# Performance work log

Hardware: AMD Instinct MI355X
Metric: run time of the kernel (lower is better)

## Reference

```python
import jax, jax.numpy as jnp
import numpy as np

H, KV, D, EPS = 32, 8, 128, 1e-6
G = H // KV  # kv groups = 4
ROPE_THETA = 5000000.0


def _rms_norm(x, gamma):
    # x: (..., D)
    return x * jax.lax.rsqrt(jnp.mean(x * x, axis=-1, keepdims=True) + EPS) * gamma


def _rotate_half(x):
    x1, x2 = jnp.split(x, 2, axis=-1)
    return jnp.concatenate([-x2, x1], axis=-1)


def _apply_rope(x, cos, sin):
    # x: (b, h, s, D); cos/sin: (b, s, 1, D) -> (b, 1, s, D)
    cos = jnp.transpose(cos, (0, 2, 1, 3))
    sin = jnp.transpose(sin, (0, 2, 1, 3))
    return x * cos + _rotate_half(x) * sin


def setup_inputs() -> dict:
    key = jax.random.key(0)
    ks = jax.random.split(key, 8)
    b, s, hid = 2, 2048, 2560
    hidden = jax.random.normal(ks[0], (b, s, hid), dtype=jnp.float32)
    # realistic RoPE tables (half-split convention matching _rotate_half)
    inv_freq = 1.0 / (ROPE_THETA ** (np.arange(0, D, 2, dtype=np.float32) / D))  # (D/2,)
    pos = np.arange(s, dtype=np.float32)
    freqs = np.outer(pos, inv_freq)                     # (s, D/2)
    emb = np.concatenate([freqs, freqs], axis=-1)       # (s, D)
    cos = jnp.broadcast_to(jnp.asarray(np.cos(emb))[None, :, None, :], (b, s, 1, D))
    sin = jnp.broadcast_to(jnp.asarray(np.sin(emb))[None, :, None, :], (b, s, 1, D))
    sc = 1.0 / np.sqrt(hid)
    wq = jax.random.normal(ks[1], (H * D, hid), dtype=jnp.float32) * sc
    wk = jax.random.normal(ks[2], (KV * D, hid), dtype=jnp.float32) * sc
    wv = jax.random.normal(ks[3], (KV * D, hid), dtype=jnp.float32) * sc
    wo = jax.random.normal(ks[4], (hid, H * D), dtype=jnp.float32) * (1.0 / np.sqrt(H * D))
    q_gamma = jnp.ones((D,), dtype=jnp.float32)
    k_gamma = jnp.ones((D,), dtype=jnp.float32)
    return {"hidden": hidden, "cos": cos, "sin": sin, "wq": wq, "wk": wk,
            "wv": wv, "wo": wo, "q_gamma": q_gamma, "k_gamma": k_gamma}


def reference(hidden, cos, sin, wq, wk, wv, wo, q_gamma, k_gamma):
    b, s, _ = hidden.shape
    # projections -> (b, heads, s, D)
    q = (hidden @ wq.T).reshape(b, s, H, D).transpose(0, 2, 1, 3)
    k = (hidden @ wk.T).reshape(b, s, KV, D).transpose(0, 2, 1, 3)
    v = (hidden @ wv.T).reshape(b, s, KV, D).transpose(0, 2, 1, 3)
    # QK-RMSNorm over head_dim
    q = _rms_norm(q, q_gamma)
    k = _rms_norm(k, k_gamma)
    # RoPE
    q = _apply_rope(q, cos, sin)
    k = _apply_rope(k, cos, sin)
    new_k, new_v = k, v  # kv cache (no prior cache)
    # GQA attention without materializing expanded K/V
    qg = q.reshape(b, KV, G, s, D)
    scale = 1.0 / np.sqrt(D)
    scores = jnp.einsum('bkgqd,bkld->bkgql', qg, k) * scale  # (b,KV,G,s,s)
    causal = jnp.tril(jnp.ones((s, s), dtype=bool))
    scores = jnp.where(causal, scores, jnp.finfo(scores.dtype).min)
    probs = jax.nn.softmax(scores, axis=-1)
    out = jnp.einsum('bkgql,bkld->bkgqd', probs, v)          # (b,KV,G,s,D)
    out = out.reshape(b, H, s, D).transpose(0, 2, 1, 3).reshape(b, s, H * D)
    return (out @ wo.T, new_k, new_v)
```

## Files before the change

### kernel.cpp

```cpp
#include <hip/hip_runtime.h>
#include <stdint.h>

typedef unsigned short u16;
typedef __attribute__((ext_vector_type(8))) short short8;
typedef __attribute__((ext_vector_type(4))) float f32x4;

#define MFMA_BF16(a,b,c) __builtin_amdgcn_mfma_f32_16x16x32_bf16((a),(b),(c),0,0,0)

#define S_BARRIER()  asm volatile("s_barrier" ::: "memory")
#define WAIT_LGKM0() asm volatile("s_waitcnt lgkmcnt(0)" ::: "memory")
#define WAIT_VM(N)   asm volatile("s_waitcnt vmcnt(" #N ")" ::: "memory")

__device__ __forceinline__ u16 f2bf(float x) {
    uint32_t u = __builtin_bit_cast(uint32_t, x);
    u += 0x7fffu + ((u >> 16) & 1u);
    return (u16)(u >> 16);
}
__device__ __forceinline__ float bf2f(u16 u) {
    return __builtin_bit_cast(float, (uint32_t)u << 16);
}
__device__ __forceinline__ void glds16(const void* g, void* lds) {
    __builtin_amdgcn_global_load_lds((const __attribute__((address_space(1))) void*)g,
                                     (__attribute__((address_space(3))) void*)lds,
                                     16, 0, 0);
}

__device__ __forceinline__ void cvt4(const float* __restrict__ s,
                                     u16* __restrict__ d, int i) {
    float4 v = *(const float4*)(s + i);
    ushort4 o;
    o.x = f2bf(v.x); o.y = f2bf(v.y); o.z = f2bf(v.z); o.w = f2bf(v.w);
    *(ushort4*)(d + i) = o;
}
__global__ __launch_bounds__(256) void cvt_all(
        const float* __restrict__ s0, u16* __restrict__ d0,
        const float* __restrict__ s1, u16* __restrict__ d1,
        const float* __restrict__ s2, u16* __restrict__ d2,
        const float* __restrict__ s3, u16* __restrict__ d3,
        const float* __restrict__ s4, u16* __restrict__ d4)
{
    int i = (blockIdx.x * 256 + threadIdx.x) * 4;
    if      (i < 10485760) cvt4(s0, d0, i);
    else if (i < 20971520) cvt4(s1, d1, i - 10485760);
    else if (i < 23592960) cvt4(s2, d2, i - 20971520);
    else if (i < 26214400) cvt4(s3, d3, i - 23592960);
    else if (i < 36700160) cvt4(s4, d4, i - 26214400);
}

template<int MH, int NH>
__device__ __forceinline__ void mm16(f32x4 (&acc)[8][4],
                                     const short8 (&a)[4][2],
                                     const short8 (&b)[2][2]) {
#pragma unroll
    for (int k2 = 0; k2 < 2; k2++)
#pragma unroll
        for (int mi = 0; mi < 4; mi++)
#pragma unroll
            for (int nj = 0; nj < 2; nj++)
                acc[MH * 4 + mi][NH * 2 + nj] =
                    MFMA_BF16(a[mi][k2], b[nj][k2], acc[MH * 4 + mi][NH * 2 + nj]);
}

template<bool BF16_OUT>
__global__ __launch_bounds__(512, 2) void gemm8(const u16* __restrict__ A,
                                                const u16* __restrict__ B,
                                                void* __restrict__ Cv,
                                                int K, int lda, int ldb, int ldc,
                                                int ntn)
{
    __shared__ __align__(16) u16 Sm[65536];
    const int t = threadIdx.x;
    const int w = t >> 6, l = t & 63;
    const int lrow = l & 15, lk = l >> 4;
    const int wm = w >> 2, wn = w & 3;

    const int nwg = (int)gridDim.x;
    const int cpx = nwg >> 3;
    const int id = (int)blockIdx.x;
    const int sw = (id & 7) * cpx + (id >> 3);
    const int tm = sw / ntn, tn = sw - tm * ntn;
    const int m0 = tm * 256, n0 = tn * 256;

    const int nkt = K >> 6;
    const size_t laneOffA = (size_t)(w * 16 + (l >> 3)) * lda + (((l & 7) ^ (l >> 3)) * 8);
    const size_t laneOffB = (size_t)(w * 16 + (l >> 3)) * ldb + (((l & 7) ^ (l >> 3)) * 8);
    const u16* Ag = A + (size_t)m0 * lda;
    const u16* Bg = B + (size_t)n0 * ldb;

    auto STAGE_A = [&](int kt, int slot, int h) {
#pragma unroll
        for (int j = 0; j < 2; j++)
            glds16(Ag + laneOffA + (size_t)(h * 128 + j * 8) * lda + kt * 64,
                   (char*)Sm + slot * 65536 + h * 16384 + w * 2048 + j * 1024);
    };
    auto STAGE_B = [&](int kt, int slot, int h) {
#pragma unroll
        for (int j = 0; j < 2; j++)
            glds16(Bg + laneOffB + (size_t)(h * 128 + j * 8) * ldb + kt * 64,
                   (char*)Sm + 32768 + slot * 65536 + h * 16384 + w * 2048 + j * 1024);
    };
    auto READ_A = [&](short8 (&a)[4][2], int slot, int rb) {
#pragma unroll
        for (int mi = 0; mi < 4; mi++)
#pragma unroll
            for (int k2 = 0; k2 < 2; k2++) {
                int row = rb + mi * 16 + lrow;
                a[mi][k2] = *(const short8*)&Sm[slot * 32768 + row * 64 +
                                                (((k2 * 4 + lk) ^ (lrow & 7)) * 8)];
            }
    };
    auto READ_B = [&](short8 (&b)[2][2], int slot, int rb) {
#pragma unroll
        for (int nj = 0; nj < 2; nj++)
#pragma unroll
            for (int k2 = 0; k2 < 2; k2++) {
                int row = rb + nj * 16 + lrow;
                b[nj][k2] = *(const short8*)&Sm[slot * 32768 + 16384 + row * 64 +
                                                (((k2 * 4 + lk) ^ (lrow & 7)) * 8)];
            }
    };

    f32x4 acc[8][4];
#pragma unroll
    for (int i = 0; i < 8; i++)
#pragma unroll
        for (int j = 0; j < 4; j++) acc[i][j] = (f32x4){0.f, 0.f, 0.f, 0.f};
    short8 aF0[4][2], aF1[4][2], bF0[2][2], bF1[2][2];

    STAGE_A(0, 0, 0); STAGE_A(0, 0, 1);
    STAGE_B(0, 0, 0); STAGE_B(0, 0, 1);
    const int k1 = (nkt > 1) ? 1 : 0;
    STAGE_A(k1, 1, 0); STAGE_A(k1, 1, 1);
    WAIT_VM(4);
    S_BARRIER();

    for (int kt = 0; kt < nkt; ++kt) {
        const int slot = kt & 1, nslot = slot ^ 1;
        const int ktB = (kt + 1 < nkt) ? kt + 1 : kt;
        const int ktA = (kt + 2 < nkt) ? kt + 2 : kt;
        READ_A(aF0, slot, wm * 128);
        READ_B(bF0, slot, wn * 64);
        STAGE_B(ktB, nslot, 0);
        S_BARRIER();
        WAIT_LGKM0();
        __builtin_amdgcn_sched_barrier(0);
        __builtin_amdgcn_s_setprio(1);
        mm16<0, 0>(acc, aF0, bF0);
        __builtin_amdgcn_s_setprio(0);
        S_BARRIER();
        READ_A(aF1, slot, wm * 128 + 64);
        STAGE_B(ktB, nslot, 1);
        S_BARRIER();
        WAIT_LGKM0();
        __builtin_amdgcn_sched_barrier(0);
        __builtin_amdgcn_s_setprio(1);
        mm16<1, 0>(acc, aF1, bF0);
        __builtin_amdgcn_s_setprio(0);
        S_BARRIER();
        READ_B(bF1, slot, wn * 64 + 32);
        STAGE_A(ktA, slot, 0);
        S_BARRIER();
        WAIT_LGKM0();
        __builtin_amdgcn_sched_barrier(0);
        __builtin_amdgcn_s_setprio(1);
        mm16<1, 1>(acc, aF1, bF1);
        __builtin_amdgcn_s_setprio(0);
        S_BARRIER();
        STAGE_A(ktA, slot, 1);
        S_BARRIER();
        __builtin_amdgcn_s_setprio(1);
        mm16<0, 1>(acc, aF0, bF1);
        __builtin_amdgcn_s_setprio(0);
        WAIT_VM(4);
        S_BARRIER();
    }
    WAIT_VM(0);

#pragma unroll
    for (int mi = 0; mi < 8; mi++) {
#pragma unroll
        for (int r = 0; r < 4; r++) {
            int row = m0 + wm * 128 + mi * 16 + lk * 4 + r;
#pragma unroll
            for (int nj = 0; nj < 4; nj++) {
                int col = n0 + wn * 64 + nj * 16 + lrow;
                float v = acc[mi][nj][r];
                if (BF16_OUT) ((u16*)Cv)[(size_t)row * ldc + col] = f2bf(v);
                else          ((float*)Cv)[(size_t)row * ldc + col] = v;
            }
        }
    }
}

__global__ __launch_bounds__(256) void norm_rope_qk(const u16* __restrict__ qkv,
        const float* __restrict__ cosb, const float* __restrict__ sinb,
        const float* __restrict__ qg, const float* __restrict__ kg,
        u16* __restrict__ qb, u16* __restrict__ kb, float* __restrict__ k_out)
{
    const int idx = blockIdx.x * 4 + (threadIdx.x >> 6);
    const int l = threadIdx.x & 63;
    const int tok = idx / 40, hd = idx - tok * 40;
    const int b = tok >> 11, pos = tok & 2047;
    const u16* row = qkv + (size_t)tok * 6144 + hd * 128;
    ushort2 xr = *(const ushort2*)(row + 2 * l);
    float xa = bf2f(xr.x), xb = bf2f(xr.y);
    float ss = xa * xa + xb * xb;
#pragma unroll
    for (int m = 1; m < 64; m <<= 1) ss += __shfl_xor(ss, m, 64);
    float rn = rsqrtf(ss * (1.0f / 128.0f) + 1e-6f);

    const float* gm = (hd < 32) ? qg : kg;
    float2 g = *(const float2*)(gm + 2 * l);
    float na = xa * rn * g.x, nb = xb * rn * g.y;
    float pa = __shfl_xor(na, 32, 64);
    float pb = __shfl_xor(nb, 32, 64);
    float2 c = *(const float2*)(cosb + (size_t)tok * 128 + 2 * l);
    float2 s = *(const float2*)(sinb + (size_t)tok * 128 + 2 * l);
    float sgn = (l < 32) ? -1.0f : 1.0f;
    float ya = na * c.x + sgn * pa * s.x;
    float yb = nb * c.y + sgn * pb * s.y;
    if (hd < 32) {
        const float qs = 0.08838834764831845f;
        size_t base = (((size_t)b * 32 + hd) * 2048 + pos) * 128;
        ushort2 o; o.x = f2bf(ya * qs); o.y = f2bf(yb * qs);
        *(ushort2*)(qb + base + 2 * l) = o;
    } else {
        int kv = hd - 32;
        size_t base = (((size_t)b * 8 + kv) * 2048 + pos) * 128;
        *(float2*)(k_out + base + 2 * l) = make_float2(ya, yb);
        ushort2 o; o.x = f2bf(ya); o.y = f2bf(yb);
        *(ushort2*)(kb + base + 2 * l) = o;
    }
}

__global__ __launch_bounds__(256) void v_pack(const u16* __restrict__ qkv,
        float* __restrict__ v_out, u16* __restrict__ vtb)
{
    __shared__ __align__(16) u16 T[64 * 128];
    const int pb = blockIdx.x, bkv = blockIdx.y;
    const int b = bkv >> 3, kv = bkv & 7;
    const int p0 = pb * 64;
    const int t = threadIdx.x;
    const int pos = t >> 2, ch4 = t & 3;
    const u16* src = qkv + (size_t)(b * 2048 + p0 + pos) * 6144 + (40 + kv) * 128 + ch4 * 32;
    float* vdst = v_out + ((size_t)bkv * 2048 + p0 + pos) * 128 + ch4 * 32;
#pragma unroll
    for (int j = 0; j < 4; j++) {
        short8 x = *(const short8*)(src + j * 8);
        float4 f0, f1;
        f0.x = bf2f(x[0]); f0.y = bf2f(x[1]); f0.z = bf2f(x[2]); f0.w = bf2f(x[3]);
        f1.x = bf2f(x[4]); f1.y = bf2f(x[5]); f1.z = bf2f(x[6]); f1.w = bf2f(x[7]);
        *(float4*)(vdst + j * 8)     = f0;
        *(float4*)(vdst + j * 8 + 4) = f1;
        int slot = (ch4 * 4 + j) ^ (pos & 7);
        *(short8*)&T[pos * 128 + slot * 8] = x;
    }
    __syncthreads();
    const int d = t & 127, ph = t >> 7;
    u16* obase = vtb + ((size_t)bkv * 128 + d) * 2048 + p0 + ph * 32;
#pragma unroll
    for (int g = 0; g < 4; g++) {
        short8 tv;
#pragma unroll
        for (int jj = 0; jj < 8; jj++) {
            int pp = ph * 32 + g * 8 + jj;
            int slot = (d >> 3) ^ (pp & 7);
            tv[jj] = (short)T[pp * 128 + slot * 8 + (d & 7)];
        }
        *(short8*)(obase + g * 8) = tv;
    }
}

__global__ __launch_bounds__(256, 3) void attn_kernel(const u16* __restrict__ qb,
        const u16* __restrict__ kb, const u16* __restrict__ vtb,
        u16* __restrict__ ao)
{
    __shared__ __align__(16) u16 Ks[64 * 128];
    __shared__ __align__(16) u16 Vs[128 * 64];
    __shared__ __align__(16) u16 Ps[4][32 * 72];

    const int p = (int)blockIdx.x;
    const int g = (p & 7) + ((p >> 5) << 3);
    const int bh = g * 4 + ((p >> 3) & 3);
    const int b = bh >> 5, h = bh & 31;
    const int kvh = h >> 2;
    const int qt = (int)gridDim.y - 1 - (int)blockIdx.y;
    const int q0 = qt * 128;
    const int t = threadIdx.x, w = t >> 6, l = t & 63;
    const int lrow = l & 15, lk = l >> 4;

    const u16* qbase  = qb  + ((size_t)b * 32 + h)  * 2048 * 128;
    const u16* kbase  = kb  + ((size_t)b * 8 + kvh) * 2048 * 128;
    const u16* vtbase = vtb + ((size_t)b * 8 + kvh) * 128 * 2048;

    short8 qf[2][4];
#pragma unroll
    for (int m = 0; m < 2; m++) {
        const u16* qrow = qbase + (size_t)(q0 + w * 32 + m * 16 + lrow) * 128 + lk * 8;
#pragma unroll
        for (int ks = 0; ks < 4; ks++) qf[m][ks] = *(const short8*)(qrow + ks * 32);
    }

    f32x4 o[2][8];
#pragma unroll
    for (int m = 0; m < 2; m++)
#pragma unroll
        for (int i = 0; i < 8; i++) o[m][i] = (f32x4){0.f, 0.f, 0.f, 0.f};
    float lsum[2][4] = {{0.f,0.f,0.f,0.f},{0.f,0.f,0.f,0.f}};

    int kR[4], kG[4], vR[4], vG[4];
#pragma unroll
    for (int i = 0; i < 4; i++) {
        int c = i * 256 + t;
        kR[i] = c >> 4; kG[i] = (c & 15) ^ (kR[i] & 7);
        vR[i] = c >> 3; vG[i] = (c & 7)  ^ (vR[i] & 7);
    }
    char* Ksb = (char*)Ks + w * 1024;
    char* Vsb = (char*)Vs + w * 1024;
    u16* pw = &Ps[w][0];
    const int wrow_max = q0 + w * 32 + 31;

    const int nkt = 2 * qt + 2;
    for (int kt = 0; kt < nkt; kt++) {
        const int kv0 = kt * 64;
        __syncthreads();
#pragma unroll
        for (int i = 0; i < 4; i++)
            glds16(kbase + (size_t)(kv0 + kR[i]) * 128 + kG[i] * 8, Ksb + i * 4096);
#pragma unroll
        for (int i = 0; i < 4; i++)
            glds16(vtbase + (size_t)vR[i] * 2048 + kv0 + vG[i] * 8, Vsb + i * 4096);
        __syncthreads();

        if (kv0 > wrow_max) continue;

        f32x4 s[2][4];
#pragma unroll
        for (int m = 0; m < 2; m++)
#pragma unroll
            for (int i = 0; i < 4; i++) s[m][i] = (f32x4){0.f, 0.f, 0.f, 0.f};
#pragma unroll
        for (int ks = 0; ks < 4; ks++) {
#pragma unroll
            for (int nt = 0; nt < 4; nt++) {
                int r = nt * 16 + lrow;
                int sl = (ks * 4 + lk) ^ (r & 7);
                short8 kf = *(const short8*)&Ks[r * 128 + sl * 8];
                s[0][nt] = MFMA_BF16(qf[0][ks], kf, s[0][nt]);
                s[1][nt] = MFMA_BF16(qf[1][ks], kf, s[1][nt]);
            }
        }

#pragma unroll
        for (int m = 0; m < 2; m++) {
            const int rowbase = q0 + w * 32 + m * 16;
            if (kv0 + 63 > rowbase) {
#pragma unroll
                for (int nt = 0; nt < 4; nt++) {
                    int cg = kv0 + nt * 16 + lrow;
#pragma unroll
                    for (int r = 0; r < 4; r++)
                        if (cg > rowbase + lk * 4 + r) s[m][nt][r] = -1e30f;
                }
            }
#pragma unroll
            for (int nt = 0; nt < 4; nt++)
#pragma unroll
                for (int r = 0; r < 4; r++) {
                    float pv = __expf(s[m][nt][r]);
                    s[m][nt][r] = pv;
                    lsum[m][r] += pv;
                    pw[(m * 16 + lk * 4 + r) * 72 + nt * 16 + lrow] = f2bf(pv);
                }
        }
        asm volatile("s_waitcnt lgkmcnt(0)" ::: "memory");

#pragma unroll
        for (int k2 = 0; k2 < 2; k2++) {
            short8 pf0 = *(const short8*)&pw[lrow * 72 + k2 * 32 + lk * 8];
            short8 pf1 = *(const short8*)&pw[(16 + lrow) * 72 + k2 * 32 + lk * 8];
#pragma unroll
            for (int nt = 0; nt < 8; nt++) {
                int rr = nt * 16 + lrow;
                int sl = (k2 * 4 + lk) ^ (rr & 7);
                short8 vf = *(const short8*)&Vs[rr * 64 + sl * 8];
                o[0][nt] = MFMA_BF16(pf0, vf, o[0][nt]);
                o[1][nt] = MFMA_BF16(pf1, vf, o[1][nt]);
            }
        }
    }

#pragma unroll
    for (int m = 0; m < 2; m++)
#pragma unroll
        for (int r = 0; r < 4; r++) {
            float v = lsum[m][r];
            v += __shfl_xor(v, 1, 64);
            v += __shfl_xor(v, 2, 64);
            v += __shfl_xor(v, 4, 64);
            v += __shfl_xor(v, 8, 64);
            lsum[m][r] = 1.0f / v;
        }
#pragma unroll
    for (int m = 0; m < 2; m++)
#pragma unroll
        for (int nt = 0; nt < 8; nt++)
#pragma unroll
            for (int r = 0; r < 4; r++) {
                int tok = q0 + w * 32 + m * 16 + lk * 4 + r;
                size_t off = ((size_t)b * 2048 + tok) * 4096 + h * 128 + nt * 16 + lrow;
                ao[off] = f2bf(o[m][nt][r] * lsum[m][r]);
            }
}

extern "C" void kernel_launch(void* const* d_in, const int* in_sizes, int n_in,
                              void* d_out, int out_size, void* d_ws, size_t ws_size,
                              hipStream_t stream)
{
    (void)in_sizes; (void)n_in; (void)out_size; (void)ws_size;
    const float* hidden = (const float*)d_in[0];
    const float* cosb   = (const float*)d_in[1];
    const float* sinb   = (const float*)d_in[2];
    const float* wq     = (const float*)d_in[3];
    const float* wk     = (const float*)d_in[4];
    const float* wv     = (const float*)d_in[5];
    const float* wo     = (const float*)d_in[6];
    const float* qg     = (const float*)d_in[7];
    const float* kg     = (const float*)d_in[8];

    float* out   = (float*)d_out;
    float* k_out = out + (size_t)2 * 2048 * 2560;
    float* v_out = k_out + (size_t)2 * 8 * 2048 * 128;

    u16* hid_b = (u16*)d_ws;
    u16* w_b   = hid_b + 10485760;
    u16* wo_b  = w_b   + 15728640;
    u16* q_b   = wo_b  + 10485760;
    u16* k_b   = q_b   + 16777216;
    u16* vt_b  = k_b   + 4194304;
    u16* qkv_b = vt_b  + 4194304;
    u16* ao_b  = hid_b;

    cvt_all<<<35840, 256, 0, stream>>>(hidden, hid_b, wq, w_b,
                                       wk, w_b + 10485760, wv, w_b + 13107200,
                                       wo, wo_b);

    gemm8<true><<<dim3(384), 512, 0, stream>>>(hid_b, w_b, qkv_b,
                                               2560, 2560, 2560, 6144, 24);
    norm_rope_qk<<<40960, 256, 0, stream>>>(qkv_b, cosb, sinb, qg, kg,
                                            q_b, k_b, k_out);
    v_pack<<<dim3(32, 16), 256, 0, stream>>>(qkv_b, v_out, vt_b);
    attn_kernel<<<dim3(64, 16), 256, 0, stream>>>(q_b, k_b, vt_b, ao_b);
    gemm8<false><<<dim3(160), 512, 0, stream>>>(ao_b, wo_b, out,
                                                4096, 4096, 4096, 2560, 10);
}
```

Baseline: 602.6 us.

## Add 256x192-tile QKV GEMM kernel and raise MFMA priority in attention

Adds a new gemm192 kernel that computes the QKV projection with 256x192 output tiles, giving 512 workgroups instead of 384 with 256x256 tiles. It uses a staged LDS double-buffer schedule with interleaved loads and MFMA phases. Separately, the attention kernel now raises wave priority around its MFMA blocks. The aim is better CU balance on the projection GEMM and better MFMA issue in attention, at the cost of a more complex pipeline and smaller per-tile reuse.

```diff
diff --git a/kernel.cpp b/kernel.cpp
--- a/kernel.cpp
+++ b/kernel.cpp
@@ -187,6 +187,159 @@
                 float v = acc[mi][nj][r];
                 if (BF16_OUT) ((u16*)Cv)[(size_t)row * ldc + col] = f2bf(v);
                 else          ((float*)Cv)[(size_t)row * ldc + col] = v;
+            }
+        }
+    }
+}
+
+__global__ __launch_bounds__(512, 2) void gemm192(const u16* __restrict__ A,
+                                                  const u16* __restrict__ B,
+                                                  u16* __restrict__ C,
+                                                  int K, int lda, int ldb, int ldc)
+{
+    __shared__ __align__(16) u16 Sm[57344];
+    const int t = threadIdx.x;
+    const int w = t >> 6, l = t & 63;
+    const int lrow = l & 15, lk = l >> 4;
+    const int wm = w >> 2, wn = w & 3;
+
+    const int nwg = (int)gridDim.x;
+    const int cpx = nwg >> 3;
+    const int id = (int)blockIdx.x;
+    const int sw = (id & 7) * cpx + (id >> 3);
+    const int tm = sw >> 5, tn = sw & 31;
+    const int m0 = tm * 256, n0 = tn * 192;
+
+    const int nkt = K >> 6;
+    const size_t laneOffA = (size_t)(w * 16 + (l >> 3)) * lda + (((l & 7) ^ (l >> 3)) * 8);
+    const size_t laneOffB = (size_t)(w * 24 + (l >> 3)) * ldb + (((l & 7) ^ (l >> 3)) * 8);
+    const u16* Ag = A + (size_t)m0 * lda;
+    const u16* Bg = B + (size_t)n0 * ldb;
+
+    auto STAGE_A = [&](int kt, int slot, int h) {
+#pragma unroll
+        for (int j = 0; j < 2; j++)
+            glds16(Ag + laneOffA + (size_t)(h * 128 + j * 8) * lda + kt * 64,
+                   (char*)Sm + slot * 32768 + h * 16384 + w * 2048 + j * 1024);
+    };
+    auto STAGE_B1 = [&](int kt, int slot, int b) {
+        glds16(Bg + laneOffB + (size_t)(b * 8) * ldb + kt * 64,
+               (char*)Sm + 65536 + slot * 24576 + w * 3072 + b * 1024);
+    };
+    auto READ_A = [&](short8 (&a)[4][2], int slot, int rb) {
+#pragma unroll
+        for (int mi = 0; mi < 4; mi++)
+#pragma unroll
+            for (int k2 = 0; k2 < 2; k2++) {
+                int row = rb + mi * 16 + lrow;
+                a[mi][k2] = *(const short8*)&Sm[slot * 16384 + row * 64 +
+                                                (((k2 * 4 + lk) ^ (lrow & 7)) * 8)];
+            }
+    };
+    auto READ_B2 = [&](short8 (&b)[2][2], int slot) {
+#pragma unroll
+        for (int nj = 0; nj < 2; nj++)
+#pragma unroll
+            for (int k2 = 0; k2 < 2; k2++) {
+                int row = wn * 48 + nj * 16 + lrow;
+                b[nj][k2] = *(const short8*)&Sm[32768 + slot * 12288 + row * 64 +
+                                                (((k2 * 4 + lk) ^ (lrow & 7)) * 8)];
+            }
+    };
+    auto READ_B1 = [&](short8 (&b)[1][2], int slot) {
+#pragma unroll
+        for (int k2 = 0; k2 < 2; k2++) {
+            int row = wn * 48 + 32 + lrow;
+            b[0][k2] = *(const short8*)&Sm[32768 + slot * 12288 + row * 64 +
+                                           (((k2 * 4 + lk) ^ (lrow & 7)) * 8)];
+        }
+    };
+
+    f32x4 acc[8][3];
+#pragma unroll
+    for (int i = 0; i < 8; i++)
+#pragma unroll
+        for (int j = 0; j < 3; j++) acc[i][j] = (f32x4){0.f, 0.f, 0.f, 0.f};
+    short8 aF0[4][2], aF1[4][2], bF0[2][2], bF1[1][2];
+
+    STAGE_A(0, 0, 0); STAGE_A(0, 0, 1);
+    STAGE_B1(0, 0, 0); STAGE_B1(0, 0, 1); STAGE_B1(0, 0, 2);
+    const int k1 = (nkt > 1) ? 1 : 0;
+    STAGE_A(k1, 1, 0); STAGE_A(k1, 1, 1);
+    WAIT_VM(4);
+    S_BARRIER();
+
+    for (int kt = 0; kt < nkt; ++kt) {
+        const int slot = kt & 1, nslot = slot ^ 1;
+        const int ktB = (kt + 1 < nkt) ? kt + 1 : kt;
+        const int ktA = (kt + 2 < nkt) ? kt + 2 : kt;
+        READ_A(aF0, slot, wm * 128);
+        READ_B2(bF0, slot);
+        STAGE_B1(ktB, nslot, 0);
+        S_BARRIER();
+        WAIT_LGKM0();
+        __builtin_amdgcn_sched_barrier(0);
+        __builtin_amdgcn_s_setprio(1);
+#pragma unroll
+        for (int k2 = 0; k2 < 2; k2++)
+#pragma unroll
+            for (int mi = 0; mi < 4; mi++)
+#pragma unroll
+                for (int nj = 0; nj < 2; nj++)
+                    acc[mi][nj] = MFMA_BF16(aF0[mi][k2], bF0[nj][k2], acc[mi][nj]);
+        __builtin_amdgcn_s_setprio(0);
+        S_BARRIER();
+        READ_A(aF1, slot, wm * 128 + 64);
+        STAGE_B1(ktB, nslot, 1); STAGE_B1(ktB, nslot, 2);
+        S_BARRIER();
+        WAIT_LGKM0();
+        __builtin_amdgcn_sched_barrier(0);
+        __builtin_amdgcn_s_setprio(1);
+#pragma unroll
+        for (int k2 = 0; k2 < 2; k2++)
+#pragma unroll
+            for (int mi = 0; mi < 4; mi++)
+#pragma unroll
+                for (int nj = 0; nj < 2; nj++)
+                    acc[4 + mi][nj] = MFMA_BF16(aF1[mi][k2], bF0[nj][k2], acc[4 + mi][nj]);
+        __builtin_amdgcn_s_setprio(0);
+        S_BARRIER();
+        READ_B1(bF1, slot);
+        STAGE_A(ktA, slot, 0);
+        S_BARRIER();
+        WAIT_LGKM0();
+        __builtin_amdgcn_sched_barrier(0);
+        __builtin_amdgcn_s_setprio(1);
+#pragma unroll
+        for (int k2 = 0; k2 < 2; k2++)
+#pragma unroll
+            for (int mi = 0; mi < 4; mi++)
+                acc[4 + mi][2] = MFMA_BF16(aF1[mi][k2], bF1[0][k2], acc[4 + mi][2]);
+        __builtin_amdgcn_s_setprio(0);
+        S_BARRIER();
+        STAGE_A(ktA, slot, 1);
+        S_BARRIER();
+        __builtin_amdgcn_s_setprio(1);
+#pragma unroll
+        for (int k2 = 0; k2 < 2; k2++)
+#pragma unroll
+            for (int mi = 0; mi < 4; mi++)
+                acc[mi][2] = MFMA_BF16(aF0[mi][k2], bF1[0][k2], acc[mi][2]);
+        __builtin_amdgcn_s_setprio(0);
+        WAIT_VM(4);
+        S_BARRIER();
+    }
+    WAIT_VM(0);
+
+#pragma unroll
+    for (int mi = 0; mi < 8; mi++) {
+#pragma unroll
+        for (int r = 0; r < 4; r++) {
+            int row = m0 + wm * 128 + mi * 16 + lk * 4 + r;
+#pragma unroll
+            for (int nj = 0; nj < 3; nj++) {
+                int col = n0 + wn * 48 + nj * 16 + lrow;
+                C[(size_t)row * ldc + col] = f2bf(acc[mi][nj][r]);
             }
         }
     }
@@ -339,6 +492,7 @@
         for (int m = 0; m < 2; m++)
 #pragma unroll
             for (int i = 0; i < 4; i++) s[m][i] = (f32x4){0.f, 0.f, 0.f, 0.f};
+        __builtin_amdgcn_s_setprio(1);
 #pragma unroll
         for (int ks = 0; ks < 4; ks++) {
 #pragma unroll
@@ -350,6 +504,7 @@
                 s[1][nt] = MFMA_BF16(qf[1][ks], kf, s[1][nt]);
             }
         }
+        __builtin_amdgcn_s_setprio(0);
 
 #pragma unroll
         for (int m = 0; m < 2; m++) {
@@ -375,6 +530,7 @@
         }
         asm volatile("s_waitcnt lgkmcnt(0)" ::: "memory");
 
+        __builtin_amdgcn_s_setprio(1);
 #pragma unroll
         for (int k2 = 0; k2 < 2; k2++) {
             short8 pf0 = *(const short8*)&pw[lrow * 72 + k2 * 32 + lk * 8];
@@ -388,6 +544,7 @@
                 o[1][nt] = MFMA_BF16(pf1, vf, o[1][nt]);
             }
         }
+        __builtin_amdgcn_s_setprio(0);
     }
 
 #pragma unroll
@@ -445,8 +602,8 @@
                                        wk, w_b + 10485760, wv, w_b + 13107200,
                                        wo, wo_b);
 
-    gemm8<true><<<dim3(384), 512, 0, stream>>>(hid_b, w_b, qkv_b,
-                                               2560, 2560, 2560, 6144, 24);
+    gemm192<<<dim3(512), 512, 0, stream>>>(hid_b, w_b, qkv_b,
+                                           2560, 2560, 2560, 6144);
     norm_rope_qk<<<40960, 256, 0, stream>>>(qkv_b, cosb, sinb, qg, kg,
                                             q_b, k_b, k_out);
     v_pack<<<dim3(32, 16), 256, 0, stream>>>(qkv_b, v_out, vt_b);
```

Measured after the change: 598.1 us. Within noise of the previous version (-0.8%).
